# Performance work log

Hardware: AMD Instinct MI355X
Metric: run time of the kernel (lower is better)

Reference implementation:

```python
import jax, jax.numpy as jnp
import numpy as np
from jax import lax

B, L, D_IN, H, RES, BD, D_OUT = 1024, 128, 5, 64, 256, 8, 1


def setup_inputs() -> dict:
    key = jax.random.key(0)
    ks = jax.random.split(key, 14)
    f = jnp.float32
    d = {}
    d["V_noise"] = jax.random.normal(ks[0], (B, D_IN), f)
    d["increments"] = jax.random.normal(ks[1], (B, L, BD), f)
    d["W1"] = jax.random.normal(ks[2], (H, D_IN), f) / np.float32(np.sqrt(D_IN))
    d["b1"] = jnp.zeros((H,), f)
    d["W2"] = jax.random.normal(ks[3], (RES, H), f) / np.float32(np.sqrt(H))
    d["b2"] = jnp.zeros((RES,), f)
    d["rho1"] = jax.random.normal(ks[4], (1, 1), f)
    d["rho2"] = jax.random.normal(ks[5], (1, 1), f)
    d["rho3"] = jax.random.normal(ks[6], (1, 1), f)
    d["rho4"] = jax.random.normal(ks[7], (1, 1), f)
    d["rho5"] = jax.random.normal(ks[8], (1, 1), f)
    # scale reservoir matrices by 1/sqrt(res) so pre-activations are O(1)
    d["B1"] = jax.random.normal(ks[9], (RES, RES), f) / np.float32(np.sqrt(RES))
    d["B2"] = jax.random.normal(ks[10], (BD, RES, RES), f) / np.float32(np.sqrt(RES))
    d["lambda1"] = jax.random.normal(ks[11], (RES, 1), f)
    d["lambda2"] = jax.random.normal(ks[12], (BD, RES, 1), f)
    d["Wr"] = jax.random.normal(ks[13], (D_OUT, RES), f) / np.float32(np.sqrt(RES))
    d["br"] = jnp.zeros((D_OUT,), f)
    return d


def reference(V_noise, increments, W1, b1, W2, b2,
              rho1, rho2, rho3, rho4, rho5,
              B1, B2, lambda1, lambda2, Wr, br):
    act = jnp.tanh
    # initial-condition MLP: [B, D_in] -> [B, RES]
    V = act(V_noise @ W1.T + b1) @ W2.T + b2
    # Brownian path with W[:,0] = 0
    Wp = jnp.cumsum(increments, axis=1).at[:, 0, :].set(0.0)
    dW = Wp[:, 1:] - Wp[:, :-1]          # [B, L-1, BD]
    l1 = lambda1[:, 0]                    # [RES]
    l2 = lambda2[:, :, 0]                 # [BD, RES]
    rho5s = rho5[0, 0]

    def step(r, dw):                      # r: [B, RES], dw: [B, BD]
        drift = act(rho1 * (r @ B1.T) + rho2 * l1)                      # [B, RES]
        diff = act(rho3 * jnp.einsum('kij,bj->bki', B2, r) + rho4 * l2)  # [B, BD, RES]
        rn = r + drift + rho5s * jnp.einsum('bki,bk->bi', diff, dw)
        return rn, rn

    _, Rs = lax.scan(step, V, jnp.swapaxes(dW, 0, 1))  # [L-1, B, RES]
    Rall = jnp.concatenate([V[None], Rs], axis=0)       # [L, B, RES]
    # time-homogeneous linear readout per lag, concatenated along time
    x = Rall @ Wr.T + br                                 # [L, B, D_out]
    out = jnp.transpose(x, (1, 0, 2)).reshape(V.shape[0], Rall.shape[0] * x.shape[-1], 1)
    return out
```

## Files before the change

### kernel.cpp

```cpp
#include <hip/hip_runtime.h>
#include <hip/hip_bf16.h>

#define B_TOT 1024
#define L_T   128
#define DIN   5
#define HD    64
#define RESN  256
#define BDN   8
#define NMAT  9
#define NROWS (NMAT * RESN)
#define PLANE ((size_t)NROWS * RESN)
#define NGRP  16
#define BG    64
#define FPB   16
#define NTHR  256
#define RB_GRP (2 * BG * RESN)
#define WS_RB_OFF  (2 * PLANE * 2)
#define WS_FLAG_OFF (WS_RB_OFF + (size_t)NGRP * RB_GRP * 4)
#define FLAGS_PER_GRP 1024

typedef __attribute__((ext_vector_type(8))) short bf16x8;
typedef __attribute__((ext_vector_type(4))) float f32x4;

__device__ __forceinline__ float fast_tanh(float x) {
    float e = __expf(2.0f * x);
    return 1.0f - 2.0f * __builtin_amdgcn_rcpf(e + 1.0f);
}

__device__ __forceinline__ unsigned pack_hilo(float v) {
    __hip_bfloat16 hi = __float2bfloat16(v);
    __hip_bfloat16 lo = __float2bfloat16(v - __bfloat162float(hi));
    return (unsigned)__builtin_bit_cast(unsigned short, hi) |
           ((unsigned)__builtin_bit_cast(unsigned short, lo) << 16);
}

__device__ __forceinline__ uint4 mall_load4(const unsigned* p) {
    uint4 r;
    asm volatile("global_load_dwordx4 %0, %1, off sc0 sc1" : "=v"(r) : "v"(p));
    return r;
}
__device__ __forceinline__ unsigned mall_load1(const unsigned* p) {
    unsigned r;
    asm volatile("global_load_dword %0, %1, off sc0 sc1" : "=v"(r) : "v"(p));
    return r;
}
__device__ __forceinline__ void mall_store1(unsigned* p, unsigned v) {
    asm volatile("global_store_dword %0, %1, off sc0 sc1" :: "v"(p), "v"(v) : "memory");
}
__device__ __forceinline__ void wait_vm0() {
    asm volatile("s_waitcnt vmcnt(0)" ::: "memory");
}

__device__ __forceinline__ void spin_all(const unsigned* fladdr, unsigned want) {
    unsigned guard = 0;
    for (;;) {
        unsigned fv = mall_load1(fladdr);
        wait_vm0();
        if (__ballot(fv < want) == 0ull) break;
        __builtin_amdgcn_s_sleep(1);
        if (++guard > (1u << 20)) break;
    }
}

__global__ void conv_w(const float* __restrict__ B1, const float* __restrict__ B2,
                       __hip_bfloat16* __restrict__ wh, __hip_bfloat16* __restrict__ wl) {
    int idx = blockIdx.x * 256 + threadIdx.x;
    float v = (idx < RESN * RESN) ? B1[idx] : B2[idx - RESN * RESN];
    __hip_bfloat16 h = __float2bfloat16(v);
    wh[idx] = h;
    wl[idx] = __float2bfloat16(v - __bfloat162float(h));
}

__global__ __launch_bounds__(NTHR, 1) void sde_ws(
    const float* __restrict__ Vn,  const float* __restrict__ inc,
    const float* __restrict__ W1,  const float* __restrict__ b1,
    const float* __restrict__ W2,  const float* __restrict__ b2,
    const float* __restrict__ rho1p, const float* __restrict__ rho2p,
    const float* __restrict__ rho3p, const float* __restrict__ rho4p,
    const float* __restrict__ rho5p,
    const float* __restrict__ lam1, const float* __restrict__ lam2,
    const float* __restrict__ Wr,  const float* __restrict__ brp,
    const __hip_bfloat16* __restrict__ wbf,
    unsigned int* __restrict__ rbu,
    unsigned int* __restrict__ flags,
    float* __restrict__ out)
{
    __shared__ __align__(16) short wlds[2][NMAT][8][64][8];
    __shared__ __align__(16) short wrlds[2][8][4][8];
    __shared__ __align__(16) short zfrag[8];

    const int tid  = threadIdx.x;
    const int mt   = tid >> 6;
    const int lane = tid & 63;
    const int n16  = lane & 15;
    const int quad = lane >> 4;
    const int bx   = blockIdx.x;
    const int g    = ((bx & 7) << 1) | (bx >> 7);
    const int fb   = (bx >> 3) & 15;
    const int f0   = fb * FPB;
    const int b0g  = g * BG;
    unsigned int* rbg    = rbu + (size_t)g * RB_GRP;
    unsigned int* flagp  = flags + g * FLAGS_PER_GRP;
    unsigned int* myflag = flagp + (fb * 4 + mt) * 16;
    const unsigned* fladdr = (const unsigned*)(flagp + ((lane & 15) * 4 + mt) * 16);

    const float rho1 = rho1p[0], rho2 = rho2p[0], rho3 = rho3p[0],
                rho4 = rho4p[0], rho5 = rho5p[0];
    const float brv = brp[0];

    float* hf  = (float*)&wlds[0][0][0][0][0];
    float* vsh = hf + 64 * 66;
    for (int p = tid; p < BG * HD; p += NTHR) {
        int b = p >> 6, hh = p & 63;
        float s = b1[hh];
        #pragma unroll
        for (int d = 0; d < DIN; ++d) s += Vn[(b0g + b) * DIN + d] * W1[hh * DIN + d];
        hf[b * 66 + hh] = fast_tanh(s);
    }
    __syncthreads();
    {
        int b = 16 * mt + (lane >> 2);
        #pragma unroll
        for (int i = 0; i < 4; ++i) {
            int f = (lane & 3) * 4 + i;
            float s = b2[f0 + f];
            #pragma unroll 8
            for (int hh = 0; hh < HD; ++hh) s += hf[b * 66 + hh] * W2[(f0 + f) * HD + hh];
            vsh[b * 16 + f] = s;
            mall_store1(&rbg[(0 * BG + b) * RESN + f0 + f], pack_hilo(s));
        }
    }
    wait_vm0();
    if (lane == 0)
        __hip_atomic_fetch_add(myflag, 1u, __ATOMIC_RELAXED, __HIP_MEMORY_SCOPE_AGENT);

    float rmast[4];
    #pragma unroll
    for (int rg = 0; rg < 4; ++rg) rmast[rg] = vsh[(16 * mt + 4 * quad + rg) * 16 + n16];
    const float l1c = lam1[f0 + n16];
    float l2c[BDN];
    #pragma unroll
    for (int k = 0; k < BDN; ++k) l2c[k] = lam2[k * RESN + f0 + n16];
    __syncthreads();

    for (int e = tid; e < 2 * NMAT * 8 * 64; e += NTHR) {
        int l  = e & 63;
        int kk = (e >> 6) & 7;
        int m  = e >> 9;
        int pl = (m >= NMAT) ? 1 : 0;
        int nt = m - pl * NMAT;
        const uint4* src = (const uint4*)(wbf + (size_t)pl * PLANE +
            (size_t)(nt * RESN + f0 + (l & 15)) * RESN + kk * 32 + (l >> 4) * 8);
        *(uint4*)&wlds[pl][nt][kk][l][0] = *src;
    }
    for (int p = tid; p < 512; p += NTHR) {
        int s = p >> 3, j = p & 7;
        int pl = s >> 5, kk = (s >> 2) & 7, q = s & 3;
        float v = Wr[kk * 32 + q * 8 + j];
        __hip_bfloat16 hi = __float2bfloat16(v);
        wrlds[pl][kk][q][j] = pl ? __builtin_bit_cast(short, __float2bfloat16(v - __bfloat162float(hi)))
                                 : __builtin_bit_cast(short, hi);
    }
    if (tid < 8) zfrag[tid] = 0;
    __syncthreads();

    const short* ph = (n16 == 0) ? &wrlds[0][0][quad][0] : &zfrag[0];
    const short* pw = (n16 == 0) ? &wrlds[1][0][quad][0] : &zfrag[0];
    const int    stp = (n16 == 0) ? 4 * 8 : 0;

    for (int t = 0; t < L_T - 1; ++t) {
        float dwv[4][8];
        #pragma unroll
        for (int rg = 0; rg < 4; ++rg) {
            const size_t bglob = (size_t)(b0g + 16 * mt + 4 * quad + rg) * (L_T * BDN);
            const float4 d0 = *(const float4*)(inc + bglob + (size_t)(t + 1) * BDN);
            const float4 d1 = *(const float4*)(inc + bglob + (size_t)(t + 1) * BDN + 4);
            dwv[rg][0] = d0.x; dwv[rg][1] = d0.y; dwv[rg][2] = d0.z; dwv[rg][3] = d0.w;
            dwv[rg][4] = d1.x; dwv[rg][5] = d1.y; dwv[rg][6] = d1.z; dwv[rg][7] = d1.w;
            if (t == 0) {
                const float4 e0 = *(const float4*)(inc + bglob);
                const float4 e1 = *(const float4*)(inc + bglob + 4);
                dwv[rg][0] += e0.x; dwv[rg][1] += e0.y; dwv[rg][2] += e0.z; dwv[rg][3] += e0.w;
                dwv[rg][4] += e1.x; dwv[rg][5] += e1.y; dwv[rg][6] += e1.z; dwv[rg][7] += e1.w;
            }
        }
        spin_all(fladdr, (unsigned)(t + 1));
        const int cur = t & 1, nxt = cur ^ 1;
        const int lead = t & 15;

        uint4 ua[16];
        {
            const unsigned* rbc = rbg + (size_t)(cur * BG + 16 * mt + n16) * RESN + quad * 8;
            #pragma unroll
            for (int kk = 0; kk < 8; ++kk) {
                ua[2 * kk]     = mall_load4(rbc + kk * 32);
                ua[2 * kk + 1] = mall_load4(rbc + kk * 32 + 4);
            }
        }
        wait_vm0();
        bf16x8 afh[8], afl[8];
        #pragma unroll
        for (int kk = 0; kk < 8; ++kk) {
            const uint4 a = ua[2 * kk], b = ua[2 * kk + 1];
            unsigned hw[4], lw[4];
            hw[0] = __builtin_amdgcn_perm(a.y, a.x, 0x05040100u);
            hw[1] = __builtin_amdgcn_perm(a.w, a.z, 0x05040100u);
            hw[2] = __builtin_amdgcn_perm(b.y, b.x, 0x05040100u);
            hw[3] = __builtin_amdgcn_perm(b.w, b.z, 0x05040100u);
            lw[0] = __builtin_amdgcn_perm(a.y, a.x, 0x07060302u);
            lw[1] = __builtin_amdgcn_perm(a.w, a.z, 0x07060302u);
            lw[2] = __builtin_amdgcn_perm(b.y, b.x, 0x07060302u);
            lw[3] = __builtin_amdgcn_perm(b.w, b.z, 0x07060302u);
            afh[kk] = __builtin_bit_cast(bf16x8, *(__attribute__((ext_vector_type(4))) unsigned*)hw);
            afl[kk] = __builtin_bit_cast(bf16x8, *(__attribute__((ext_vector_type(4))) unsigned*)lw);
        }

        f32x4 acc[NMAT] = {};
        #pragma unroll
        for (int kk = 0; kk < 8; ++kk) {
            bf16x8 bh[NMAT], bl[NMAT];
            #pragma unroll
            for (int nt = 0; nt < NMAT; ++nt) {
                bh[nt] = *(const bf16x8*)&wlds[0][nt][kk][lane][0];
                bl[nt] = *(const bf16x8*)&wlds[1][nt][kk][lane][0];
            }
            #pragma unroll
            for (int nt = 0; nt < NMAT; ++nt)
                acc[nt] = __builtin_amdgcn_mfma_f32_16x16x32_bf16(afh[kk], bh[nt], acc[nt], 0, 0, 0);
            #pragma unroll
            for (int nt = 0; nt < NMAT; ++nt)
                acc[nt] = __builtin_amdgcn_mfma_f32_16x16x32_bf16(afl[kk], bh[nt], acc[nt], 0, 0, 0);
            #pragma unroll
            for (int nt = 0; nt < NMAT; ++nt)
                acc[nt] = __builtin_amdgcn_mfma_f32_16x16x32_bf16(afh[kk], bl[nt], acc[nt], 0, 0, 0);
        }

        #pragma unroll
        for (int rg = 0; rg < 4; ++rg) {
            const int bl_ = 16 * mt + 4 * quad + rg;
            float drift = fast_tanh(rho1 * acc[0][rg] + rho2 * l1c);
            float s = 0.0f;
            #pragma unroll
            for (int k = 0; k < BDN; ++k)
                s += fast_tanh(rho3 * acc[1 + k][rg] + rho4 * l2c[k]) * dwv[rg][k];
            float rn = rmast[rg] + drift + rho5 * s;
            rmast[rg] = rn;
            mall_store1(&rbg[(nxt * BG + bl_) * RESN + f0 + n16], pack_hilo(rn));
        }
        wait_vm0();
        if (lane == 0)
            __hip_atomic_fetch_add(myflag, 1u, __ATOMIC_RELAXED, __HIP_MEMORY_SCOPE_AGENT);

        if (fb == lead) {
            f32x4 accw = {};
            #pragma unroll
            for (int kk = 0; kk < 8; ++kk) {
                bf16x8 wh8 = *(const bf16x8*)(ph + kk * stp);
                bf16x8 wl8 = *(const bf16x8*)(pw + kk * stp);
                accw = __builtin_amdgcn_mfma_f32_16x16x32_bf16(afh[kk], wh8, accw, 0, 0, 0);
                accw = __builtin_amdgcn_mfma_f32_16x16x32_bf16(afl[kk], wh8, accw, 0, 0, 0);
                accw = __builtin_amdgcn_mfma_f32_16x16x32_bf16(afh[kk], wl8, accw, 0, 0, 0);
            }
            if (n16 == 0) {
                #pragma unroll
                for (int rg = 0; rg < 4; ++rg)
                    out[(size_t)(b0g + 16 * mt + 4 * quad + rg) * L_T + t] = accw[rg] + brv;
            }
        }
    }

    if (fb == 15) {
        spin_all(fladdr, (unsigned)L_T);
        uint4 ua[16];
        const unsigned* rbc = rbg + (size_t)(1 * BG + 16 * mt + n16) * RESN + quad * 8;
        #pragma unroll
        for (int kk = 0; kk < 8; ++kk) {
            ua[2 * kk]     = mall_load4(rbc + kk * 32);
            ua[2 * kk + 1] = mall_load4(rbc + kk * 32 + 4);
        }
        wait_vm0();
        f32x4 accw = {};
        #pragma unroll
        for (int kk = 0; kk < 8; ++kk) {
            const uint4 a = ua[2 * kk], b = ua[2 * kk + 1];
            unsigned hw[4], lw[4];
            hw[0] = __builtin_amdgcn_perm(a.y, a.x, 0x05040100u);
            hw[1] = __builtin_amdgcn_perm(a.w, a.z, 0x05040100u);
            hw[2] = __builtin_amdgcn_perm(b.y, b.x, 0x05040100u);
            hw[3] = __builtin_amdgcn_perm(b.w, b.z, 0x05040100u);
            lw[0] = __builtin_amdgcn_perm(a.y, a.x, 0x07060302u);
            lw[1] = __builtin_amdgcn_perm(a.w, a.z, 0x07060302u);
            lw[2] = __builtin_amdgcn_perm(b.y, b.x, 0x07060302u);
            lw[3] = __builtin_amdgcn_perm(b.w, b.z, 0x07060302u);
            bf16x8 ah = __builtin_bit_cast(bf16x8, *(__attribute__((ext_vector_type(4))) unsigned*)hw);
            bf16x8 al = __builtin_bit_cast(bf16x8, *(__attribute__((ext_vector_type(4))) unsigned*)lw);
            bf16x8 wh8 = *(const bf16x8*)(ph + kk * stp);
            bf16x8 wl8 = *(const bf16x8*)(pw + kk * stp);
            accw = __builtin_amdgcn_mfma_f32_16x16x32_bf16(ah, wh8, accw, 0, 0, 0);
            accw = __builtin_amdgcn_mfma_f32_16x16x32_bf16(al, wh8, accw, 0, 0, 0);
            accw = __builtin_amdgcn_mfma_f32_16x16x32_bf16(ah, wl8, accw, 0, 0, 0);
        }
        if (n16 == 0) {
            #pragma unroll
            for (int rg = 0; rg < 4; ++rg)
                out[(size_t)(b0g + 16 * mt + 4 * quad + rg) * L_T + (L_T - 1)] = accw[rg] + brv;
        }
    }
}

extern "C" void kernel_launch(void* const* d_in, const int* in_sizes, int n_in,
                              void* d_out, int out_size, void* d_ws, size_t ws_size,
                              hipStream_t stream) {
    const float* Vn   = (const float*)d_in[0];
    const float* inc  = (const float*)d_in[1];
    const float* W1   = (const float*)d_in[2];
    const float* b1   = (const float*)d_in[3];
    const float* W2   = (const float*)d_in[4];
    const float* b2   = (const float*)d_in[5];
    const float* r1   = (const float*)d_in[6];
    const float* r2   = (const float*)d_in[7];
    const float* r3   = (const float*)d_in[8];
    const float* r4   = (const float*)d_in[9];
    const float* r5   = (const float*)d_in[10];
    const float* B1   = (const float*)d_in[11];
    const float* B2   = (const float*)d_in[12];
    const float* lam1 = (const float*)d_in[13];
    const float* lam2 = (const float*)d_in[14];
    const float* Wr   = (const float*)d_in[15];
    const float* br   = (const float*)d_in[16];

    __hip_bfloat16* wh    = (__hip_bfloat16*)d_ws;
    unsigned int*   rbu   = (unsigned int*)((char*)d_ws + WS_RB_OFF);
    unsigned int*   flags = (unsigned int*)((char*)d_ws + WS_FLAG_OFF);
    float* out = (float*)d_out;

    hipMemsetAsync(flags, 0, NGRP * FLAGS_PER_GRP * sizeof(unsigned int), stream);
    conv_w<<<dim3(NROWS * RESN / 256), dim3(256), 0, stream>>>(B1, B2, wh, wh + PLANE);
    sde_ws<<<dim3(256), dim3(NTHR), 0, stream>>>(
        Vn, inc, W1, b1, W2, b2, r1, r2, r3, r4, r5, lam1, lam2, Wr, br,
        wh, rbu, flags, out);
}
```

Before: 870.0 us.

## Exchange state via XCD-local L2 when groups share an XCD, split hi/lo planes

Each block records its XCD id at launch. A group checks whether all 16 of its blocks landed on the same XCD, and if so uses L2-coherent (sc0 only) loads, stores and atomics for the per-step state exchange and flag spinning instead of bypassing to MALL. The exchange buffer is also split into separate bf16 hi and lo planes, so MFMA fragments load directly without perm repacking. The cost is a one-time global registration barrier and reliance on the scheduler placing group blocks on one XCD. Otherwise it falls back to the MALL path.

New measurement: 763.6 us. 12.2% less time.

```diff
diff --git a/kernel.cpp b/kernel.cpp
--- a/kernel.cpp
+++ b/kernel.cpp
@@ -14,9 +14,11 @@
 #define BG    64
 #define FPB   16
 #define NTHR  256
-#define RB_GRP (2 * BG * RESN)
+#define RB_GRP_BYTES (2 * BG * RESN * 4)
+#define BUF_SHORTS (BG * RESN)
+#define LO_OFF     (2 * BUF_SHORTS)
 #define WS_RB_OFF  (2 * PLANE * 2)
-#define WS_FLAG_OFF (WS_RB_OFF + (size_t)NGRP * RB_GRP * 4)
+#define WS_FLAG_OFF (WS_RB_OFF + (size_t)NGRP * RB_GRP_BYTES)
 #define FLAGS_PER_GRP 1024
 
 typedef __attribute__((ext_vector_type(8))) short bf16x8;
@@ -27,34 +29,52 @@
     return 1.0f - 2.0f * __builtin_amdgcn_rcpf(e + 1.0f);
 }
 
-__device__ __forceinline__ unsigned pack_hilo(float v) {
-    __hip_bfloat16 hi = __float2bfloat16(v);
-    __hip_bfloat16 lo = __float2bfloat16(v - __bfloat162float(hi));
-    return (unsigned)__builtin_bit_cast(unsigned short, hi) |
-           ((unsigned)__builtin_bit_cast(unsigned short, lo) << 16);
-}
-
-__device__ __forceinline__ uint4 mall_load4(const unsigned* p) {
-    uint4 r;
-    asm volatile("global_load_dwordx4 %0, %1, off sc0 sc1" : "=v"(r) : "v"(p));
-    return r;
-}
+__device__ __forceinline__ void split_hl(float v, unsigned short& h, unsigned short& l) {
+    __hip_bfloat16 hb = __float2bfloat16(v);
+    h = __builtin_bit_cast(unsigned short, hb);
+    l = __builtin_bit_cast(unsigned short, __float2bfloat16(v - __bfloat162float(hb)));
+}
+
 __device__ __forceinline__ unsigned mall_load1(const unsigned* p) {
     unsigned r;
     asm volatile("global_load_dword %0, %1, off sc0 sc1" : "=v"(r) : "v"(p));
     return r;
 }
+__device__ __forceinline__ unsigned l2_load1(const unsigned* p) {
+    unsigned r;
+    asm volatile("global_load_dword %0, %1, off sc0" : "=v"(r) : "v"(p));
+    return r;
+}
 __device__ __forceinline__ void mall_store1(unsigned* p, unsigned v) {
     asm volatile("global_store_dword %0, %1, off sc0 sc1" :: "v"(p), "v"(v) : "memory");
 }
+__device__ __forceinline__ uint4 mall_load4s(const unsigned short* p) {
+    uint4 r;
+    asm volatile("global_load_dwordx4 %0, %1, off sc0 sc1" : "=v"(r) : "v"(p));
+    return r;
+}
+__device__ __forceinline__ uint4 l2_load4s(const unsigned short* p) {
+    uint4 r;
+    asm volatile("global_load_dwordx4 %0, %1, off sc0" : "=v"(r) : "v"(p));
+    return r;
+}
+__device__ __forceinline__ void mall_store2(unsigned short* p, unsigned v) {
+    asm volatile("global_store_short %0, %1, off sc0 sc1" :: "v"(p), "v"(v) : "memory");
+}
+__device__ __forceinline__ void l2_store2(unsigned short* p, unsigned v) {
+    asm volatile("global_store_short %0, %1, off sc0" :: "v"(p), "v"(v) : "memory");
+}
+__device__ __forceinline__ void atom_add_l2(unsigned* p, unsigned v) {
+    asm volatile("global_atomic_add %0, %1, off" :: "v"(p), "v"(v) : "memory");
+}
 __device__ __forceinline__ void wait_vm0() {
     asm volatile("s_waitcnt vmcnt(0)" ::: "memory");
 }
 
-__device__ __forceinline__ void spin_all(const unsigned* fladdr, unsigned want) {
+__device__ __forceinline__ void spin_all(const unsigned* fladdr, unsigned want, bool l2m) {
     unsigned guard = 0;
     for (;;) {
-        unsigned fv = mall_load1(fladdr);
+        unsigned fv = l2m ? l2_load1(fladdr) : mall_load1(fladdr);
         wait_vm0();
         if (__ballot(fv < want) == 0ull) break;
         __builtin_amdgcn_s_sleep(1);
@@ -81,13 +101,14 @@
     const float* __restrict__ lam1, const float* __restrict__ lam2,
     const float* __restrict__ Wr,  const float* __restrict__ brp,
     const __hip_bfloat16* __restrict__ wbf,
-    unsigned int* __restrict__ rbu,
+    unsigned short* __restrict__ rbs,
     unsigned int* __restrict__ flags,
     float* __restrict__ out)
 {
     __shared__ __align__(16) short wlds[2][NMAT][8][64][8];
     __shared__ __align__(16) short wrlds[2][8][4][8];
     __shared__ __align__(16) short zfrag[8];
+    __shared__ int l2mode_sh;
 
     const int tid  = threadIdx.x;
     const int mt   = tid >> 6;
@@ -99,10 +120,20 @@
     const int fb   = (bx >> 3) & 15;
     const int f0   = fb * FPB;
     const int b0g  = g * BG;
-    unsigned int* rbg    = rbu + (size_t)g * RB_GRP;
+    unsigned short* gbs = rbs + (size_t)g * (RB_GRP_BYTES / 2);
     unsigned int* flagp  = flags + g * FLAGS_PER_GRP;
     unsigned int* myflag = flagp + (fb * 4 + mt) * 16;
     const unsigned* fladdr = (const unsigned*)(flagp + ((lane & 15) * 4 + mt) * 16);
+    unsigned* regtbl = flags + NGRP * FLAGS_PER_GRP;
+    unsigned* regcnt = regtbl + 256;
+
+    if (tid == 0) {
+        unsigned xcd;
+        asm volatile("s_getreg_b32 %0, hwreg(HW_REG_XCC_ID)" : "=s"(xcd));
+        mall_store1(&regtbl[bx], xcd);
+        wait_vm0();
+        __hip_atomic_fetch_add(regcnt, 1u, __ATOMIC_RELAXED, __HIP_MEMORY_SCOPE_AGENT);
+    }
 
     const float rho1 = rho1p[0], rho2 = rho2p[0], rho3 = rho3p[0],
                 rho4 = rho4p[0], rho5 = rho5p[0];
@@ -118,8 +149,31 @@
         hf[b * 66 + hh] = fast_tanh(s);
     }
     __syncthreads();
+
+    if (tid == 0) {
+        unsigned cnt, guard = 0;
+        do {
+            cnt = mall_load1(regcnt);
+            wait_vm0();
+            if (cnt >= 256) break;
+            __builtin_amdgcn_s_sleep(1);
+        } while (++guard < (1u << 22));
+        unsigned e[16];
+        #pragma unroll
+        for (int q = 0; q < 16; ++q)
+            e[q] = mall_load1(&regtbl[((g & 1) << 7) | (q << 3) | (g >> 1)]);
+        wait_vm0();
+        int ok = (cnt >= 256) ? 1 : 0;
+        #pragma unroll
+        for (int q = 1; q < 16; ++q) ok &= (e[q] == e[0]) ? 1 : 0;
+        l2mode_sh = ok;
+    }
+    __syncthreads();
+    const bool l2m = (l2mode_sh != 0);
+
     {
         int b = 16 * mt + (lane >> 2);
+        float sv[4];
         #pragma unroll
         for (int i = 0; i < 4; ++i) {
             int f = (lane & 3) * 4 + i;
@@ -127,12 +181,33 @@
             #pragma unroll 8
             for (int hh = 0; hh < HD; ++hh) s += hf[b * 66 + hh] * W2[(f0 + f) * HD + hh];
             vsh[b * 16 + f] = s;
-            mall_store1(&rbg[(0 * BG + b) * RESN + f0 + f], pack_hilo(s));
+            sv[i] = s;
+        }
+        unsigned short hs[4], ls[4];
+        #pragma unroll
+        for (int i = 0; i < 4; ++i) split_hl(sv[i], hs[i], ls[i]);
+        unsigned short* pb = gbs + b * 256 + f0;
+        if (l2m) {
+            #pragma unroll
+            for (int i = 0; i < 4; ++i) {
+                int f = (lane & 3) * 4 + i;
+                l2_store2(pb + f, hs[i]);
+                l2_store2(pb + f + LO_OFF, ls[i]);
+            }
+        } else {
+            #pragma unroll
+            for (int i = 0; i < 4; ++i) {
+                int f = (lane & 3) * 4 + i;
+                mall_store2(pb + f, hs[i]);
+                mall_store2(pb + f + LO_OFF, ls[i]);
+            }
         }
     }
     wait_vm0();
-    if (lane == 0)
-        __hip_atomic_fetch_add(myflag, 1u, __ATOMIC_RELAXED, __HIP_MEMORY_SCOPE_AGENT);
+    if (lane == 0) {
+        if (l2m) atom_add_l2(myflag, 1u);
+        else __hip_atomic_fetch_add(myflag, 1u, __ATOMIC_RELAXED, __HIP_MEMORY_SCOPE_AGENT);
+    }
 
     float rmast[4];
     #pragma unroll
@@ -184,36 +259,28 @@
                 dwv[rg][4] += e1.x; dwv[rg][5] += e1.y; dwv[rg][6] += e1.z; dwv[rg][7] += e1.w;
             }
         }
-        spin_all(fladdr, (unsigned)(t + 1));
+        spin_all(fladdr, (unsigned)(t + 1), l2m);
         const int cur = t & 1, nxt = cur ^ 1;
         const int lead = t & 15;
 
-        uint4 ua[16];
+        bf16x8 afh[8], afl[8];
         {
-            const unsigned* rbc = rbg + (size_t)(cur * BG + 16 * mt + n16) * RESN + quad * 8;
-            #pragma unroll
-            for (int kk = 0; kk < 8; ++kk) {
-                ua[2 * kk]     = mall_load4(rbc + kk * 32);
-                ua[2 * kk + 1] = mall_load4(rbc + kk * 32 + 4);
-            }
-        }
-        wait_vm0();
-        bf16x8 afh[8], afl[8];
-        #pragma unroll
-        for (int kk = 0; kk < 8; ++kk) {
-            const uint4 a = ua[2 * kk], b = ua[2 * kk + 1];
-            unsigned hw[4], lw[4];
-            hw[0] = __builtin_amdgcn_perm(a.y, a.x, 0x05040100u);
-            hw[1] = __builtin_amdgcn_perm(a.w, a.z, 0x05040100u);
-            hw[2] = __builtin_amdgcn_perm(b.y, b.x, 0x05040100u);
-            hw[3] = __builtin_amdgcn_perm(b.w, b.z, 0x05040100u);
-            lw[0] = __builtin_amdgcn_perm(a.y, a.x, 0x07060302u);
-            lw[1] = __builtin_amdgcn_perm(a.w, a.z, 0x07060302u);
-            lw[2] = __builtin_amdgcn_perm(b.y, b.x, 0x07060302u);
-            lw[3] = __builtin_amdgcn_perm(b.w, b.z, 0x07060302u);
-            afh[kk] = __builtin_bit_cast(bf16x8, *(__attribute__((ext_vector_type(4))) unsigned*)hw);
-            afl[kk] = __builtin_bit_cast(bf16x8, *(__attribute__((ext_vector_type(4))) unsigned*)lw);
-        }
+            const unsigned short* pc = gbs + cur * BUF_SHORTS + (16 * mt + n16) * 256 + quad * 8;
+            if (l2m) {
+                #pragma unroll
+                for (int kk = 0; kk < 8; ++kk) {
+                    afh[kk] = __builtin_bit_cast(bf16x8, l2_load4s(pc + kk * 32));
+                    afl[kk] = __builtin_bit_cast(bf16x8, l2_load4s(pc + kk * 32 + LO_OFF));
+                }
+            } else {
+                #pragma unroll
+                for (int kk = 0; kk < 8; ++kk) {
+                    afh[kk] = __builtin_bit_cast(bf16x8, mall_load4s(pc + kk * 32));
+                    afl[kk] = __builtin_bit_cast(bf16x8, mall_load4s(pc + kk * 32 + LO_OFF));
+                }
+            }
+        }
+        wait_vm0();
 
         f32x4 acc[NMAT] = {};
         #pragma unroll
@@ -235,9 +302,9 @@
                 acc[nt] = __builtin_amdgcn_mfma_f32_16x16x32_bf16(afh[kk], bl[nt], acc[nt], 0, 0, 0);
         }
 
+        unsigned short hs[4], ls[4];
         #pragma unroll
         for (int rg = 0; rg < 4; ++rg) {
-            const int bl_ = 16 * mt + 4 * quad + rg;
             float drift = fast_tanh(rho1 * acc[0][rg] + rho2 * l1c);
             float s = 0.0f;
             #pragma unroll
@@ -245,11 +312,31 @@
                 s += fast_tanh(rho3 * acc[1 + k][rg] + rho4 * l2c[k]) * dwv[rg][k];
             float rn = rmast[rg] + drift + rho5 * s;
             rmast[rg] = rn;
-            mall_store1(&rbg[(nxt * BG + bl_) * RESN + f0 + n16], pack_hilo(rn));
-        }
-        wait_vm0();
-        if (lane == 0)
-            __hip_atomic_fetch_add(myflag, 1u, __ATOMIC_RELAXED, __HIP_MEMORY_SCOPE_AGENT);
+            split_hl(rn, hs[rg], ls[rg]);
+        }
+        {
+            unsigned short* pb = gbs + nxt * BUF_SHORTS + f0 + n16;
+            if (l2m) {
+                #pragma unroll
+                for (int rg = 0; rg < 4; ++rg) {
+                    const int bl_ = 16 * mt + 4 * quad + rg;
+                    l2_store2(pb + bl_ * 256, hs[rg]);
+                    l2_store2(pb + bl_ * 256 + LO_OFF, ls[rg]);
+                }
+            } else {
+                #pragma unroll
+                for (int rg = 0; rg < 4; ++rg) {
+                    const int bl_ = 16 * mt + 4 * quad + rg;
+                    mall_store2(pb + bl_ * 256, hs[rg]);
+                    mall_store2(pb + bl_ * 256 + LO_OFF, ls[rg]);
+                }
+            }
+        }
+        wait_vm0();
+        if (lane == 0) {
+            if (l2m) atom_add_l2(myflag, 1u);
+            else __hip_atomic_fetch_add(myflag, 1u, __ATOMIC_RELAXED, __HIP_MEMORY_SCOPE_AGENT);
+        }
 
         if (fb == lead) {
             f32x4 accw = {};
@@ -270,35 +357,33 @@
     }
 
     if (fb == 15) {
-        spin_all(fladdr, (unsigned)L_T);
-        uint4 ua[16];
-        const unsigned* rbc = rbg + (size_t)(1 * BG + 16 * mt + n16) * RESN + quad * 8;
+        spin_all(fladdr, (unsigned)L_T, l2m);
+        bf16x8 ah[8], al[8];
+        {
+            const unsigned short* pc = gbs + 1 * BUF_SHORTS + (16 * mt + n16) * 256 + quad * 8;
+            if (l2m) {
+                #pragma unroll
+                for (int kk = 0; kk < 8; ++kk) {
+                    ah[kk] = __builtin_bit_cast(bf16x8, l2_load4s(pc + kk * 32));
+                    al[kk] = __builtin_bit_cast(bf16x8, l2_load4s(pc + kk * 32 + LO_OFF));
+                }
+            } else {
+                #pragma unroll
+                for (int kk = 0; kk < 8; ++kk) {
+                    ah[kk] = __builtin_bit_cast(bf16x8, mall_load4s(pc + kk * 32));
+                    al[kk] = __builtin_bit_cast(bf16x8, mall_load4s(pc + kk * 32 + LO_OFF));
+                }
+            }
+        }
+        wait_vm0();
+        f32x4 accw = {};
         #pragma unroll
         for (int kk = 0; kk < 8; ++kk) {
-            ua[2 * kk]     = mall_load4(rbc + kk * 32);
-            ua[2 * kk + 1] = mall_load4(rbc + kk * 32 + 4);
-        }
-        wait_vm0();
-        f32x4 accw = {};
-        #pragma unroll
-        for (int kk = 0; kk < 8; ++kk) {
-            const uint4 a = ua[2 * kk], b = ua[2 * kk + 1];
-            unsigned hw[4], lw[4];
-            hw[0] = __builtin_amdgcn_perm(a.y, a.x, 0x05040100u);
-            hw[1] = __builtin_amdgcn_perm(a.w, a.z, 0x05040100u);
-            hw[2] = __builtin_amdgcn_perm(b.y, b.x, 0x05040100u);
-            hw[3] = __builtin_amdgcn_perm(b.w, b.z, 0x05040100u);
-            lw[0] = __builtin_amdgcn_perm(a.y, a.x, 0x07060302u);
-            lw[1] = __builtin_amdgcn_perm(a.w, a.z, 0x07060302u);
-            lw[2] = __builtin_amdgcn_perm(b.y, b.x, 0x07060302u);
-            lw[3] = __builtin_amdgcn_perm(b.w, b.z, 0x07060302u);
-            bf16x8 ah = __builtin_bit_cast(bf16x8, *(__attribute__((ext_vector_type(4))) unsigned*)hw);
-            bf16x8 al = __builtin_bit_cast(bf16x8, *(__attribute__((ext_vector_type(4))) unsigned*)lw);
             bf16x8 wh8 = *(const bf16x8*)(ph + kk * stp);
             bf16x8 wl8 = *(const bf16x8*)(pw + kk * stp);
-            accw = __builtin_amdgcn_mfma_f32_16x16x32_bf16(ah, wh8, accw, 0, 0, 0);
-            accw = __builtin_amdgcn_mfma_f32_16x16x32_bf16(al, wh8, accw, 0, 0, 0);
-            accw = __builtin_amdgcn_mfma_f32_16x16x32_bf16(ah, wl8, accw, 0, 0, 0);
+            accw = __builtin_amdgcn_mfma_f32_16x16x32_bf16(ah[kk], wh8, accw, 0, 0, 0);
+            accw = __builtin_amdgcn_mfma_f32_16x16x32_bf16(al[kk], wh8, accw, 0, 0, 0);
+            accw = __builtin_amdgcn_mfma_f32_16x16x32_bf16(ah[kk], wl8, accw, 0, 0, 0);
         }
         if (n16 == 0) {
             #pragma unroll
@@ -330,13 +415,13 @@
     const float* br   = (const float*)d_in[16];
 
     __hip_bfloat16* wh    = (__hip_bfloat16*)d_ws;
-    unsigned int*   rbu   = (unsigned int*)((char*)d_ws + WS_RB_OFF);
+    unsigned short* rbs   = (unsigned short*)((char*)d_ws + WS_RB_OFF);
     unsigned int*   flags = (unsigned int*)((char*)d_ws + WS_FLAG_OFF);
     float* out = (float*)d_out;
 
-    hipMemsetAsync(flags, 0, NGRP * FLAGS_PER_GRP * sizeof(unsigned int), stream);
+    hipMemsetAsync(flags, 0, NGRP * FLAGS_PER_GRP * sizeof(unsigned int) + 2048, stream);
     conv_w<<<dim3(NROWS * RESN / 256), dim3(256), 0, stream>>>(B1, B2, wh, wh + PLANE);
     sde_ws<<<dim3(256), dim3(NTHR), 0, stream>>>(
         Vn, inc, W1, b1, W2, b2, r1, r2, r3, r4, r5, lam1, lam2, Wr, br,
-        wh, rbu, flags, out);
-}
+        wh, rbs, flags, out);
+}
```
